# Kernel optimization log

Measured on AMD Instinct MI355X. Metric: run time of the kernel, lower is better.

The kernel has to match this reference:

```python
import jax, jax.numpy as jnp
import numpy as np

TEMPERATURE = 1.0
NUM_EXPERTS = 8


def setup_inputs() -> dict:
    key = jax.random.key(0)
    ks = jax.random.split(key, 7)
    B, S, H, E = 4, 4096, 1024, NUM_EXPERTS
    scale = 1.0 / np.sqrt(H)
    return {
        "hidden_states": jax.random.normal(ks[0], (B, S, H), dtype=jnp.float32),
        "w1": jax.random.normal(ks[1], (H, H // 2), dtype=jnp.float32) * scale,
        "b1": jax.random.normal(ks[2], (H // 2,), dtype=jnp.float32) * 0.01,
        "w2": jax.random.normal(ks[3], (H // 2, E), dtype=jnp.float32) * (1.0 / np.sqrt(H // 2)),
        "b2": jax.random.normal(ks[4], (E,), dtype=jnp.float32) * 0.01,
        "expert_W": jax.random.normal(ks[5], (E, H, H), dtype=jnp.float32) * scale,
        "expert_b": jax.random.normal(ks[6], (E, H), dtype=jnp.float32) * 0.01,
    }


def reference(hidden_states, w1, b1, w2, b2, expert_W, expert_b):
    # Router MLP: Linear(H, H//2) -> ReLU -> Linear(H//2, E)  (dropout inactive at eval)
    h = jax.nn.relu(jnp.einsum("bsh,hm->bsm", hidden_states, w1) + b1)
    routing_scores = (jnp.einsum("bsm,me->bse", h, w2) + b2) / TEMPERATURE
    expert_probs = jax.nn.softmax(routing_scores, axis=-1)
    # top-1 routing (topk with k=1 == argmax of probs)
    top_idx = jnp.argmax(expert_probs, axis=-1)  # [B, S]
    onehot = jax.nn.one_hot(top_idx, NUM_EXPERTS, dtype=hidden_states.dtype)  # [B, S, E]

    # _apply_expert_routing: for each expert, masked input -> dense transform -> masked accumulate
    routed = jnp.zeros_like(hidden_states)
    for e in range(NUM_EXPERTS):
        mask = onehot[..., e:e + 1]  # [B, S, 1]
        expert_out = jnp.einsum("bsh,hd->bsd", hidden_states * mask, expert_W[e]) + expert_b[e]
        routed = routed + expert_out * mask
    return routed
```

## Files before the change

### kernel.cpp

```cpp
#include <hip/hip_runtime.h>

#define NTOK 16384
#define HDIM 1024
#define MDIM 512
#define NEXP 8
#define CHUNK 128
#define MAXCHUNK 136
#define RCAP 4096
#define DELTA 0.02f
#define LSTR 72

#define G1_NWG ((MDIM / 128) * (NTOK / 128))
#define EG_NWG (8 * MAXCHUNK)

typedef __bf16 bf16x8 __attribute__((ext_vector_type(8)));
typedef float floatx4 __attribute__((ext_vector_type(4)));

__device__ __forceinline__ void gll16(const void* g, void* l) {
  __builtin_amdgcn_global_load_lds(
      (const __attribute__((address_space(1))) void*)g,
      (__attribute__((address_space(3))) void*)l, 16, 0, 0);
}

__global__ __launch_bounds__(256) void cvt_hs(
    const float* __restrict__ src, __bf16* __restrict__ dst)
{
  const size_t i = ((size_t)blockIdx.x * 256 + threadIdx.x) * 8;
  float4 a = *(const float4*)&src[i];
  float4 b = *(const float4*)&src[i + 4];
  bf16x8 o;
  o[0] = (__bf16)a.x; o[1] = (__bf16)a.y; o[2] = (__bf16)a.z; o[3] = (__bf16)a.w;
  o[4] = (__bf16)b.x; o[5] = (__bf16)b.y; o[6] = (__bf16)b.z; o[7] = (__bf16)b.w;
  *(bf16x8*)&dst[i] = o;
}

__global__ __launch_bounds__(256) void transpose_cvt(
    const float* __restrict__ src, __bf16* __restrict__ dst, int K, int C)
{
  __shared__ __align__(16) __bf16 T[64 * LSTR];
  const int b = blockIdx.z;
  const int k0 = blockIdx.x * 64, c0 = blockIdx.y * 64;
  const float* S = src + (size_t)b * K * C;
  __bf16* D = dst + (size_t)b * K * C;
  const int t = threadIdx.x;
  {
    const int r = t >> 2, cc = (t & 3) * 16;
    const float* p = S + (size_t)(k0 + r) * C + c0 + cc;
    float4 v0 = *(const float4*)&p[0];
    float4 v1 = *(const float4*)&p[4];
    float4 v2 = *(const float4*)&p[8];
    float4 v3 = *(const float4*)&p[12];
    float vv[16] = {v0.x, v0.y, v0.z, v0.w, v1.x, v1.y, v1.z, v1.w,
                    v2.x, v2.y, v2.z, v2.w, v3.x, v3.y, v3.z, v3.w};
#pragma unroll
    for (int j = 0; j < 16; ++j) T[(cc + j) * LSTR + r] = (__bf16)vv[j];
  }
  __syncthreads();
  {
    const int c = t >> 2, kk = (t & 3) * 16;
    __bf16* q = D + (size_t)(c0 + c) * K + k0 + kk;
    *(float4*)&q[0] = *(const float4*)&T[c * LSTR + kk];
    *(float4*)&q[8] = *(const float4*)&T[c * LSTR + kk + 8];
  }
}

__global__ __launch_bounds__(256) void gemm1_score(
    const __bf16* __restrict__ A,
    const __bf16* __restrict__ Bt,
    const float* __restrict__ bias,
    const float* __restrict__ w2,
    float* __restrict__ scores_part)
{
  __shared__ __align__(16) __bf16 As[2 * 128 * 64];
  __shared__ __align__(16) __bf16 Bs[2 * 128 * 64];

  const int tid = threadIdx.x;
  const int swz = (blockIdx.x & 7) * (G1_NWG / 8) + (blockIdx.x >> 3);
  const int rowBlk = swz >> 2;
  const int cb = swz & 3;
  const int row0 = rowBlk * 128, col0 = cb * 128;
  const int wave = tid >> 6, lane = tid & 63;
  const int lrow8 = lane >> 3;
  const int gchunk = (lane & 7) ^ lrow8;
  const int wr = (wave >> 1) * 64, wc = (wave & 1) * 64;
  const int lrow = lane & 15, quad = lane >> 4;

  const __bf16 *pa[4], *pb[4];
#pragma unroll
  for (int p = 0; p < 4; ++p) {
    const int rb = wave * 8 + p * 32;
    pa[p] = A + (size_t)(row0 + rb + lrow8) * HDIM + gchunk * 8;
    pb[p] = Bt + (size_t)(col0 + rb + lrow8) * HDIM + gchunk * 8;
  }

  floatx4 acc[4][4];
#pragma unroll
  for (int i = 0; i < 4; ++i)
#pragma unroll
    for (int j = 0; j < 4; ++j) acc[i][j] = (floatx4){0.f, 0.f, 0.f, 0.f};

#pragma unroll
  for (int p = 0; p < 4; ++p) {
    const int rb = wave * 8 + p * 32;
    gll16(pa[p], &As[rb * 64]);
    gll16(pb[p], &Bs[rb * 64]);
  }
  __syncthreads();

  int cur = 0;
  for (int t = 0; t < HDIM / 64; ++t) {
    const int nxt = cur ^ 1;
    if (t + 1 < HDIM / 64) {
      const int koff = (t + 1) * 64;
#pragma unroll
      for (int p = 0; p < 4; ++p) {
        const int rb = wave * 8 + p * 32;
        gll16(pa[p] + koff, &As[nxt * 8192 + rb * 64]);
        gll16(pb[p] + koff, &Bs[nxt * 8192 + rb * 64]);
      }
    }
    const __bf16* Ab = &As[cur * 8192];
    const __bf16* Bb = &Bs[cur * 8192];
#pragma unroll
    for (int kh = 0; kh < 2; ++kh) {
      bf16x8 a[4], b[4];
#pragma unroll
      for (int i = 0; i < 4; ++i)
        a[i] = *(const bf16x8*)&Ab[(wr + i * 16 + lrow) * 64 +
                                   (((kh * 4 + quad) ^ (lrow & 7)) * 8)];
#pragma unroll
      for (int j = 0; j < 4; ++j)
        b[j] = *(const bf16x8*)&Bb[(wc + j * 16 + lrow) * 64 +
                                   (((kh * 4 + quad) ^ (lrow & 7)) * 8)];
#pragma unroll
      for (int i = 0; i < 4; ++i)
#pragma unroll
        for (int j = 0; j < 4; ++j)
          acc[i][j] = __builtin_amdgcn_mfma_f32_16x16x32_bf16(a[i], b[j], acc[i][j], 0, 0, 0);
    }
    __syncthreads();
    cur = nxt;
  }

  float* w2s = (float*)As;
  float* sblk = (float*)Bs;
  *(float4*)&w2s[tid * 4] = *(const float4*)&w2[col0 * 8 + tid * 4];
  __syncthreads();

  float bj[4];
  float4 wja[4], wjb[4];
#pragma unroll
  for (int j = 0; j < 4; ++j) {
    const int cl = wc + j * 16 + lrow;
    bj[j] = bias[col0 + cl];
    wja[j] = *(const float4*)&w2s[cl * 8];
    wjb[j] = *(const float4*)&w2s[cl * 8 + 4];
  }

#pragma unroll
  for (int i = 0; i < 4; ++i) {
#pragma unroll
    for (int r = 0; r < 4; ++r) {
      float4 sA = {0, 0, 0, 0}, sB = {0, 0, 0, 0};
#pragma unroll
      for (int j = 0; j < 4; ++j) {
        float h = fmaxf(acc[i][j][r] + bj[j], 0.f);
        sA.x += h * wja[j].x; sA.y += h * wja[j].y;
        sA.z += h * wja[j].z; sA.w += h * wja[j].w;
        sB.x += h * wjb[j].x; sB.y += h * wjb[j].y;
        sB.z += h * wjb[j].z; sB.w += h * wjb[j].w;
      }
#pragma unroll
      for (int m = 1; m <= 8; m <<= 1) {
        sA.x += __shfl_xor(sA.x, m, 64); sA.y += __shfl_xor(sA.y, m, 64);
        sA.z += __shfl_xor(sA.z, m, 64); sA.w += __shfl_xor(sA.w, m, 64);
        sB.x += __shfl_xor(sB.x, m, 64); sB.y += __shfl_xor(sB.y, m, 64);
        sB.z += __shfl_xor(sB.z, m, 64); sB.w += __shfl_xor(sB.w, m, 64);
      }
      if (lrow == 0) {
        const int rloc = wr + i * 16 + quad * 4 + r;
        *(float4*)&sblk[((wave & 1) * 128 + rloc) * 8] = sA;
        *(float4*)&sblk[((wave & 1) * 128 + rloc) * 8 + 4] = sB;
      }
    }
  }
  __syncthreads();
  {
    const int r = tid >> 1, e4 = (tid & 1) * 4;
    float4 v0 = *(const float4*)&sblk[r * 8 + e4];
    float4 v1 = *(const float4*)&sblk[(128 + r) * 8 + e4];
    float4 o = {v0.x + v1.x, v0.y + v1.y, v0.z + v1.z, v0.w + v1.w};
    *(float4*)&scores_part[((size_t)cb * NTOK + row0 + r) * 8 + e4] = o;
  }
}

__global__ __launch_bounds__(256) void routing_argmax(
    const float* __restrict__ scores_part, const float* __restrict__ b2,
    int* __restrict__ top_idx, int* __restrict__ risky_n,
    int* __restrict__ risky)
{
  __shared__ int rbuf[256];
  __shared__ int rcnt, rbase;
  if (threadIdx.x == 0) rcnt = 0;
  __syncthreads();

  const int t = blockIdx.x * 256 + threadIdx.x;
  float4 sa = {0, 0, 0, 0}, sb = {0, 0, 0, 0};
#pragma unroll
  for (int c = 0; c < 4; ++c) {
    float4 va = *(const float4*)&scores_part[((size_t)c * NTOK + t) * 8];
    float4 vb = *(const float4*)&scores_part[((size_t)c * NTOK + t) * 8 + 4];
    sa.x += va.x; sa.y += va.y; sa.z += va.z; sa.w += va.w;
    sb.x += vb.x; sb.y += vb.y; sb.z += vb.z; sb.w += vb.w;
  }
  float s[8] = {sa.x + b2[0], sa.y + b2[1], sa.z + b2[2], sa.w + b2[3],
                sb.x + b2[4], sb.y + b2[5], sb.z + b2[6], sb.w + b2[7]};
  float best = s[0], second = -1e30f;
  int bi = 0;
#pragma unroll
  for (int e = 1; e < 8; ++e) {
    if (s[e] > best) { second = best; best = s[e]; bi = e; }
    else if (s[e] > second) second = s[e];
  }
  top_idx[t] = bi;
  if (best - second < DELTA) rbuf[atomicAdd(&rcnt, 1)] = t;
  __syncthreads();
  if (threadIdx.x == 0 && rcnt > 0) rbase = atomicAdd(risky_n, rcnt);
  __syncthreads();
  if ((int)threadIdx.x < rcnt) {
    int slot = rbase + threadIdx.x;
    if (slot < RCAP) risky[slot] = rbuf[threadIdx.x];
  }
}

__global__ __launch_bounds__(256) void gemm1_fix_v2(
    const float* __restrict__ A, const float* __restrict__ W,
    const float* __restrict__ bias, const int* __restrict__ risky,
    float* __restrict__ hfix)
{
  __shared__ float As[32][33];
  __shared__ float Bs[32][64];
  __shared__ int toks[32];

  const int tid = threadIdx.x;
  if (tid < 32) toks[tid] = risky[blockIdx.y * 32 + tid];
  __syncthreads();
  if (toks[0] < 0) return;

  const int col0 = blockIdx.x * 64;
  const int tx = tid & 15, ty = tid >> 4;
  float acc0[4] = {0, 0, 0, 0}, acc1[4] = {0, 0, 0, 0};

  const int sr = tid >> 3;
  const int sc4 = (tid & 3) * 8;
  const int lo = tid & 7;
  const int sc8 = lo * 8;
  const int tokS = toks[sr];
  const float* pa = (tokS >= 0) ? A + (size_t)tokS * HDIM : A;

  for (int k0 = 0; k0 < HDIM; k0 += 32) {
    float4 av = make_float4(0, 0, 0, 0);
    if (tokS >= 0) av = *(const float4*)&pa[k0 + (lo & 3) * 4 + (lo >> 2) * 16];
    float4 b0 = *(const float4*)&W[(size_t)(k0 + sr) * MDIM + col0 + sc8];
    float4 b1v = *(const float4*)&W[(size_t)(k0 + sr) * MDIM + col0 + sc8 + 4];
    const int kk = (lo & 3) * 4 + (lo >> 2) * 16;
    As[kk + 0][sr] = av.x; As[kk + 1][sr] = av.y;
    As[kk + 2][sr] = av.z; As[kk + 3][sr] = av.w;
    (void)sc4;
    *(float4*)&Bs[sr][sc8] = b0;
    *(float4*)&Bs[sr][sc8 + 4] = b1v;
    __syncthreads();

#pragma unroll
    for (int k = 0; k < 32; ++k) {
      float a0 = As[k][ty], a1 = As[k][ty + 16];
      float4 bv = *(const float4*)&Bs[k][tx * 4];
      acc0[0] = fmaf(a0, bv.x, acc0[0]); acc0[1] = fmaf(a0, bv.y, acc0[1]);
      acc0[2] = fmaf(a0, bv.z, acc0[2]); acc0[3] = fmaf(a0, bv.w, acc0[3]);
      acc1[0] = fmaf(a1, bv.x, acc1[0]); acc1[1] = fmaf(a1, bv.y, acc1[1]);
      acc1[2] = fmaf(a1, bv.z, acc1[2]); acc1[3] = fmaf(a1, bv.w, acc1[3]);
    }
    __syncthreads();
  }

  const int c = col0 + tx * 4;
  const int i0 = blockIdx.y * 32 + ty, i1 = blockIdx.y * 32 + ty + 16;
  if (toks[ty] >= 0) {
    float4 v;
    v.x = fmaxf(acc0[0] + bias[c + 0], 0.f); v.y = fmaxf(acc0[1] + bias[c + 1], 0.f);
    v.z = fmaxf(acc0[2] + bias[c + 2], 0.f); v.w = fmaxf(acc0[3] + bias[c + 3], 0.f);
    *(float4*)&hfix[(size_t)i0 * MDIM + c] = v;
  }
  if (toks[ty + 16] >= 0) {
    float4 v;
    v.x = fmaxf(acc1[0] + bias[c + 0], 0.f); v.y = fmaxf(acc1[1] + bias[c + 1], 0.f);
    v.z = fmaxf(acc1[2] + bias[c + 2], 0.f); v.w = fmaxf(acc1[3] + bias[c + 3], 0.f);
    *(float4*)&hfix[(size_t)i1 * MDIM + c] = v;
  }
}

__global__ __launch_bounds__(256) void rescore_fix(
    const float* __restrict__ hfix, const float* __restrict__ w2,
    const float* __restrict__ b2, const int* __restrict__ risky,
    int* __restrict__ top_idx)
{
  const int idx = blockIdx.x * 32 + (threadIdx.x >> 3);
  const int l8 = threadIdx.x & 7;
  const int t = risky[idx];

  float s[8] = {0, 0, 0, 0, 0, 0, 0, 0};
  if (t >= 0) {
    const float* hrow = hfix + (size_t)idx * MDIM;
    for (int k = l8; k < MDIM; k += 8) {
      float hv = hrow[k];
      float4 wa = *(const float4*)&w2[k * 8];
      float4 wb = *(const float4*)&w2[k * 8 + 4];
      s[0] += hv * wa.x; s[1] += hv * wa.y; s[2] += hv * wa.z; s[3] += hv * wa.w;
      s[4] += hv * wb.x; s[5] += hv * wb.y; s[6] += hv * wb.z; s[7] += hv * wb.w;
    }
  }
#pragma unroll
  for (int off = 4; off > 0; off >>= 1)
#pragma unroll
    for (int e = 0; e < 8; ++e) s[e] += __shfl_xor(s[e], off, 64);

  if (l8 == 0 && t >= 0) {
    float best = s[0] + b2[0];
    int bi = 0;
#pragma unroll
    for (int e = 1; e < 8; ++e) {
      float v = s[e] + b2[e];
      if (v > best) { best = v; bi = e; }
    }
    top_idx[t] = bi;
  }
}

__global__ __launch_bounds__(256) void count_tokens(
    const int* __restrict__ top_idx, int* __restrict__ counts)
{
  __shared__ int lc[NEXP];
  if (threadIdx.x < NEXP) lc[threadIdx.x] = 0;
  __syncthreads();
  atomicAdd(&lc[top_idx[blockIdx.x * 256 + threadIdx.x]], 1);
  __syncthreads();
  if (threadIdx.x < NEXP) atomicAdd(&counts[threadIdx.x], lc[threadIdx.x]);
}

__global__ __launch_bounds__(256) void scatter_tokens(
    const int* __restrict__ top_idx, const int* __restrict__ counts,
    int* __restrict__ cursor, int* __restrict__ sorted)
{
  __shared__ int lc[NEXP], lbase[NEXP], off_s[NEXP];
  if (threadIdx.x < NEXP) lc[threadIdx.x] = 0;
  if (threadIdx.x == 0) {
    int off = 0;
    for (int e = 0; e < NEXP; ++e) {
      off_s[e] = off;
      off += ((counts[e] + CHUNK - 1) / CHUNK) * CHUNK;
    }
  }
  __syncthreads();
  const int t = blockIdx.x * 256 + threadIdx.x;
  const int e = top_idx[t];
  const int r = atomicAdd(&lc[e], 1);
  __syncthreads();
  if (threadIdx.x < NEXP)
    lbase[threadIdx.x] = atomicAdd(&cursor[threadIdx.x], lc[threadIdx.x]);
  __syncthreads();
  sorted[off_s[e] + lbase[e] + r] = t;
}

__global__ __launch_bounds__(256) void expert_gemm_v4(
    const __bf16* __restrict__ A,
    const __bf16* __restrict__ Wt,
    const float* __restrict__ Eb,
    const int* __restrict__ sorted,
    const int* __restrict__ top_idx,
    float* __restrict__ Out)
{
  __shared__ __align__(16) __bf16 As[2 * 128 * 64];
  __shared__ __align__(16) __bf16 Bs[2 * 128 * 64];
  __shared__ int toks[CHUNK];

  const int tid = threadIdx.x;
  const int swz = (blockIdx.x & 7) * (EG_NWG / 8) + (blockIdx.x >> 3);
  const int chunkIdx = swz >> 3;
  const int cb = swz & 7;
  if (tid < CHUNK) toks[tid] = sorted[(size_t)chunkIdx * CHUNK + tid];
  __syncthreads();
  if (toks[0] < 0) return;

  const int e = top_idx[toks[0]];
  const int col0 = cb * 128;
  const int wave = tid >> 6, lane = tid & 63;
  const int lrow8 = lane >> 3;
  const int gchunk = (lane & 7) ^ lrow8;
  const int wr = (wave >> 1) * 64, wc = (wave & 1) * 64;
  const int lrow = lane & 15, quad = lane >> 4;

  const __bf16 *pa[4], *pb[4];
#pragma unroll
  for (int p = 0; p < 4; ++p) {
    const int rb = wave * 8 + p * 32;
    const int tk = toks[rb + lrow8];
    pa[p] = A + (size_t)(tk < 0 ? 0 : tk) * HDIM + gchunk * 8;
    pb[p] = Wt + ((size_t)e * HDIM + col0 + rb + lrow8) * HDIM + gchunk * 8;
  }

  floatx4 acc[4][4];
#pragma unroll
  for (int i = 0; i < 4; ++i)
#pragma unroll
    for (int j = 0; j < 4; ++j) acc[i][j] = (floatx4){0.f, 0.f, 0.f, 0.f};

#pragma unroll
  for (int p = 0; p < 4; ++p) {
    const int rb = wave * 8 + p * 32;
    gll16(pa[p], &As[rb * 64]);
    gll16(pb[p], &Bs[rb * 64]);
  }
  __syncthreads();

  int cur = 0;
  for (int t = 0; t < HDIM / 64; ++t) {
    const int nxt = cur ^ 1;
    if (t + 1 < HDIM / 64) {
      const int koff = (t + 1) * 64;
#pragma unroll
      for (int p = 0; p < 4; ++p) {
        const int rb = wave * 8 + p * 32;
        gll16(pa[p] + koff, &As[nxt * 8192 + rb * 64]);
        gll16(pb[p] + koff, &Bs[nxt * 8192 + rb * 64]);
      }
    }
    const __bf16* Ab = &As[cur * 8192];
    const __bf16* Bb = &Bs[cur * 8192];
#pragma unroll
    for (int kh = 0; kh < 2; ++kh) {
      bf16x8 a[4], b[4];
#pragma unroll
      for (int i = 0; i < 4; ++i)
        a[i] = *(const bf16x8*)&Ab[(wr + i * 16 + lrow) * 64 +
                                   (((kh * 4 + quad) ^ (lrow & 7)) * 8)];
#pragma unroll
      for (int j = 0; j < 4; ++j)
        b[j] = *(const bf16x8*)&Bb[(wc + j * 16 + lrow) * 64 +
                                   (((kh * 4 + quad) ^ (lrow & 7)) * 8)];
#pragma unroll
      for (int i = 0; i < 4; ++i)
#pragma unroll
        for (int j = 0; j < 4; ++j)
          acc[i][j] = __builtin_amdgcn_mfma_f32_16x16x32_bf16(a[i], b[j], acc[i][j], 0, 0, 0);
    }
    __syncthreads();
    cur = nxt;
  }

  const float* be = Eb + (size_t)e * HDIM + col0;
#pragma unroll
  for (int i = 0; i < 4; ++i)
#pragma unroll
    for (int r = 0; r < 4; ++r) {
      const int row = wr + i * 16 + quad * 4 + r;
      const int tok = toks[row];
      if (tok < 0) continue;
      float* po = Out + (size_t)tok * HDIM + col0;
#pragma unroll
      for (int j = 0; j < 4; ++j) {
        const int col = wc + j * 16 + lrow;
        po[col] = acc[i][j][r] + be[col];
      }
    }
}

extern "C" void kernel_launch(void* const* d_in, const int* in_sizes, int n_in,
                              void* d_out, int out_size, void* d_ws, size_t ws_size,
                              hipStream_t stream) {
  (void)in_sizes; (void)n_in; (void)out_size; (void)ws_size;

  const float* hs = (const float*)d_in[0];
  const float* w1 = (const float*)d_in[1];
  const float* b1 = (const float*)d_in[2];
  const float* w2 = (const float*)d_in[3];
  const float* b2 = (const float*)d_in[4];
  const float* eW = (const float*)d_in[5];
  const float* eb = (const float*)d_in[6];
  float* out = (float*)d_out;

  float* hfix = (float*)d_out;
  float* scores_part = hfix + (size_t)RCAP * MDIM;

  char* wsb = (char*)d_ws;
  int* top_idx = (int*)wsb;
  int* ctrl    = (int*)(wsb + 65536);
  int* counts  = ctrl;
  int* risky_n = ctrl + 8;
  int* cursor  = ctrl + 16;
  int* risky   = (int*)(wsb + 65792);
  int* sorted  = risky + RCAP;
  __bf16* hs_bf = (__bf16*)(wsb + 163840);
  __bf16* w1t   = (__bf16*)(wsb + 163840 + 33554432);
  __bf16* eWt   = (__bf16*)(wsb + 163840 + 33554432 + 1048576);

  hipMemsetAsync(ctrl, 0, 128, stream);
  hipMemsetAsync(risky, 0xFF, (RCAP + MAXCHUNK * CHUNK) * sizeof(int), stream);

  cvt_hs<<<NTOK * HDIM / (256 * 8), 256, 0, stream>>>(hs, hs_bf);
  transpose_cvt<<<dim3(HDIM / 64, MDIM / 64, 1), 256, 0, stream>>>(w1, w1t, HDIM, MDIM);
  transpose_cvt<<<dim3(HDIM / 64, HDIM / 64, NEXP), 256, 0, stream>>>(eW, eWt, HDIM, HDIM);

  gemm1_score<<<dim3(G1_NWG), 256, 0, stream>>>(hs_bf, w1t, b1, w2, scores_part);
  routing_argmax<<<NTOK / 256, 256, 0, stream>>>(scores_part, b2, top_idx, risky_n, risky);
  gemm1_fix_v2<<<dim3(MDIM / 64, RCAP / 32), 256, 0, stream>>>(hs, w1, b1, risky, hfix);
  rescore_fix<<<RCAP / 32, 256, 0, stream>>>(hfix, w2, b2, risky, top_idx);
  count_tokens<<<NTOK / 256, 256, 0, stream>>>(top_idx, counts);
  scatter_tokens<<<NTOK / 256, 256, 0, stream>>>(top_idx, counts, cursor, sorted);
  expert_gemm_v4<<<dim3(EG_NWG), 256, 0, stream>>>(hs_bf, eWt, eb, sorted, top_idx, out);
}
```

Before: 326.0 us.

## Deepen GEMM pipelines to 4-stage with 512-thread blocks and split router scoring

Both bf16 GEMMs (router layer 1 and expert GEMM) move from 256-thread double-buffered tiles to 512-thread blocks with a 4-buffer LDS ring, prefetching three K-steps ahead. They use explicit vmcnt waits and a single barrier per step in place of two syncthreads. The router's fused ReLU·w2 epilogue is removed: gemm1 now writes bf16 hidden activations to scratch, and a new score_route kernel computes the scores and argmax per token. This targets memory latency and epilogue reduction cost, but adds a bf16 round-trip of the hidden activations and 128KB of LDS per block, which limits occupancy. The extra rounding of h to bf16 may shift which tokens fall in the near-tie set.

```diff
diff --git a/kernel.cpp b/kernel.cpp
--- a/kernel.cpp
+++ b/kernel.cpp
@@ -9,6 +9,7 @@
 #define RCAP 4096
 #define DELTA 0.02f
 #define LSTR 72
+#define NSTEP 16
 
 #define G1_NWG ((MDIM / 128) * (NTOK / 128))
 #define EG_NWG (8 * MAXCHUNK)
@@ -64,15 +65,14 @@
   }
 }
 
-__global__ __launch_bounds__(256) void gemm1_score(
+__global__ __launch_bounds__(512, 2) void gemm1_h(
     const __bf16* __restrict__ A,
     const __bf16* __restrict__ Bt,
     const float* __restrict__ bias,
-    const float* __restrict__ w2,
-    float* __restrict__ scores_part)
-{
-  __shared__ __align__(16) __bf16 As[2 * 128 * 64];
-  __shared__ __align__(16) __bf16 Bs[2 * 128 * 64];
+    __bf16* __restrict__ hbf)
+{
+  __shared__ __align__(16) __bf16 As[4][128 * 64];
+  __shared__ __align__(16) __bf16 Bs[4][128 * 64];
 
   const int tid = threadIdx.x;
   const int swz = (blockIdx.x & 7) * (G1_NWG / 8) + (blockIdx.x >> 3);
@@ -82,148 +82,135 @@
   const int wave = tid >> 6, lane = tid & 63;
   const int lrow8 = lane >> 3;
   const int gchunk = (lane & 7) ^ lrow8;
-  const int wr = (wave >> 1) * 64, wc = (wave & 1) * 64;
+  const int wr = (wave >> 2) * 64;
+  const int wc = (wave & 3) * 32;
   const int lrow = lane & 15, quad = lane >> 4;
 
-  const __bf16 *pa[4], *pb[4];
-#pragma unroll
-  for (int p = 0; p < 4; ++p) {
-    const int rb = wave * 8 + p * 32;
+  const __bf16 *pa[2], *pb[2];
+#pragma unroll
+  for (int p = 0; p < 2; ++p) {
+    const int rb = wave * 8 + p * 64;
     pa[p] = A + (size_t)(row0 + rb + lrow8) * HDIM + gchunk * 8;
     pb[p] = Bt + (size_t)(col0 + rb + lrow8) * HDIM + gchunk * 8;
   }
 
-  floatx4 acc[4][4];
+  floatx4 acc[4][2];
 #pragma unroll
   for (int i = 0; i < 4; ++i)
 #pragma unroll
-    for (int j = 0; j < 4; ++j) acc[i][j] = (floatx4){0.f, 0.f, 0.f, 0.f};
-
-#pragma unroll
-  for (int p = 0; p < 4; ++p) {
-    const int rb = wave * 8 + p * 32;
-    gll16(pa[p], &As[rb * 64]);
-    gll16(pb[p], &Bs[rb * 64]);
-  }
-  __syncthreads();
-
-  int cur = 0;
-  for (int t = 0; t < HDIM / 64; ++t) {
-    const int nxt = cur ^ 1;
-    if (t + 1 < HDIM / 64) {
-      const int koff = (t + 1) * 64;
-#pragma unroll
-      for (int p = 0; p < 4; ++p) {
-        const int rb = wave * 8 + p * 32;
-        gll16(pa[p] + koff, &As[nxt * 8192 + rb * 64]);
-        gll16(pb[p] + koff, &Bs[nxt * 8192 + rb * 64]);
+    for (int j = 0; j < 2; ++j) acc[i][j] = (floatx4){0.f, 0.f, 0.f, 0.f};
+
+#pragma unroll
+  for (int pt = 0; pt < 3; ++pt) {
+#pragma unroll
+    for (int p = 0; p < 2; ++p) {
+      const int rb = wave * 8 + p * 64;
+      gll16(pa[p] + pt * 64, &As[pt][rb * 64]);
+      gll16(pb[p] + pt * 64, &Bs[pt][rb * 64]);
+    }
+  }
+
+  for (int t = 0; t < NSTEP; ++t) {
+    if (t < NSTEP - 2)      asm volatile("s_waitcnt vmcnt(8)" ::: "memory");
+    else if (t == NSTEP - 2) asm volatile("s_waitcnt vmcnt(4)" ::: "memory");
+    else                     asm volatile("s_waitcnt vmcnt(0)" ::: "memory");
+    __builtin_amdgcn_s_barrier();
+    __builtin_amdgcn_sched_barrier(0);
+    if (t + 3 < NSTEP) {
+      const int koff = (t + 3) * 64;
+      const int bn = (t + 3) & 3;
+#pragma unroll
+      for (int p = 0; p < 2; ++p) {
+        const int rb = wave * 8 + p * 64;
+        gll16(pa[p] + koff, &As[bn][rb * 64]);
+        gll16(pb[p] + koff, &Bs[bn][rb * 64]);
       }
     }
-    const __bf16* Ab = &As[cur * 8192];
-    const __bf16* Bb = &Bs[cur * 8192];
+    __builtin_amdgcn_sched_barrier(0);
+    const __bf16* Ab = As[t & 3];
+    const __bf16* Bb = Bs[t & 3];
 #pragma unroll
     for (int kh = 0; kh < 2; ++kh) {
-      bf16x8 a[4], b[4];
+      bf16x8 a[4], b[2];
 #pragma unroll
       for (int i = 0; i < 4; ++i)
         a[i] = *(const bf16x8*)&Ab[(wr + i * 16 + lrow) * 64 +
                                    (((kh * 4 + quad) ^ (lrow & 7)) * 8)];
 #pragma unroll
-      for (int j = 0; j < 4; ++j)
+      for (int j = 0; j < 2; ++j)
         b[j] = *(const bf16x8*)&Bb[(wc + j * 16 + lrow) * 64 +
                                    (((kh * 4 + quad) ^ (lrow & 7)) * 8)];
 #pragma unroll
       for (int i = 0; i < 4; ++i)
 #pragma unroll
-        for (int j = 0; j < 4; ++j)
+        for (int j = 0; j < 2; ++j)
           acc[i][j] = __builtin_amdgcn_mfma_f32_16x16x32_bf16(a[i], b[j], acc[i][j], 0, 0, 0);
     }
-    __syncthreads();
-    cur = nxt;
-  }
-
-  float* w2s = (float*)As;
-  float* sblk = (float*)Bs;
-  *(float4*)&w2s[tid * 4] = *(const float4*)&w2[col0 * 8 + tid * 4];
-  __syncthreads();
-
-  float bj[4];
-  float4 wja[4], wjb[4];
-#pragma unroll
-  for (int j = 0; j < 4; ++j) {
-    const int cl = wc + j * 16 + lrow;
-    bj[j] = bias[col0 + cl];
-    wja[j] = *(const float4*)&w2s[cl * 8];
-    wjb[j] = *(const float4*)&w2s[cl * 8 + 4];
-  }
-
-#pragma unroll
-  for (int i = 0; i < 4; ++i) {
+  }
+
+  float bj[2];
+#pragma unroll
+  for (int j = 0; j < 2; ++j) bj[j] = bias[col0 + wc + j * 16 + lrow];
+#pragma unroll
+  for (int i = 0; i < 4; ++i)
 #pragma unroll
     for (int r = 0; r < 4; ++r) {
-      float4 sA = {0, 0, 0, 0}, sB = {0, 0, 0, 0};
-#pragma unroll
-      for (int j = 0; j < 4; ++j) {
-        float h = fmaxf(acc[i][j][r] + bj[j], 0.f);
-        sA.x += h * wja[j].x; sA.y += h * wja[j].y;
-        sA.z += h * wja[j].z; sA.w += h * wja[j].w;
-        sB.x += h * wjb[j].x; sB.y += h * wjb[j].y;
-        sB.z += h * wjb[j].z; sB.w += h * wjb[j].w;
+      const int tokr = row0 + wr + i * 16 + quad * 4 + r;
+      __bf16* hp = hbf + (size_t)tokr * MDIM + col0;
+#pragma unroll
+      for (int j = 0; j < 2; ++j) {
+        const int cl = wc + j * 16 + lrow;
+        hp[cl] = (__bf16)fmaxf(acc[i][j][r] + bj[j], 0.f);
       }
-#pragma unroll
-      for (int m = 1; m <= 8; m <<= 1) {
-        sA.x += __shfl_xor(sA.x, m, 64); sA.y += __shfl_xor(sA.y, m, 64);
-        sA.z += __shfl_xor(sA.z, m, 64); sA.w += __shfl_xor(sA.w, m, 64);
-        sB.x += __shfl_xor(sB.x, m, 64); sB.y += __shfl_xor(sB.y, m, 64);
-        sB.z += __shfl_xor(sB.z, m, 64); sB.w += __shfl_xor(sB.w, m, 64);
-      }
-      if (lrow == 0) {
-        const int rloc = wr + i * 16 + quad * 4 + r;
-        *(float4*)&sblk[((wave & 1) * 128 + rloc) * 8] = sA;
-        *(float4*)&sblk[((wave & 1) * 128 + rloc) * 8 + 4] = sB;
-      }
-    }
-  }
-  __syncthreads();
-  {
-    const int r = tid >> 1, e4 = (tid & 1) * 4;
-    float4 v0 = *(const float4*)&sblk[r * 8 + e4];
-    float4 v1 = *(const float4*)&sblk[(128 + r) * 8 + e4];
-    float4 o = {v0.x + v1.x, v0.y + v1.y, v0.z + v1.z, v0.w + v1.w};
-    *(float4*)&scores_part[((size_t)cb * NTOK + row0 + r) * 8 + e4] = o;
-  }
-}
-
-__global__ __launch_bounds__(256) void routing_argmax(
-    const float* __restrict__ scores_part, const float* __restrict__ b2,
-    int* __restrict__ top_idx, int* __restrict__ risky_n,
-    int* __restrict__ risky)
-{
-  __shared__ int rbuf[256];
+    }
+}
+
+__global__ __launch_bounds__(256) void score_route(
+    const __bf16* __restrict__ hbf, const float* __restrict__ w2,
+    const float* __restrict__ b2, int* __restrict__ top_idx,
+    int* __restrict__ risky_n, int* __restrict__ risky)
+{
+  __shared__ int rbuf[32];
   __shared__ int rcnt, rbase;
   if (threadIdx.x == 0) rcnt = 0;
   __syncthreads();
 
-  const int t = blockIdx.x * 256 + threadIdx.x;
-  float4 sa = {0, 0, 0, 0}, sb = {0, 0, 0, 0};
-#pragma unroll
-  for (int c = 0; c < 4; ++c) {
-    float4 va = *(const float4*)&scores_part[((size_t)c * NTOK + t) * 8];
-    float4 vb = *(const float4*)&scores_part[((size_t)c * NTOK + t) * 8 + 4];
-    sa.x += va.x; sa.y += va.y; sa.z += va.z; sa.w += va.w;
-    sb.x += vb.x; sb.y += vb.y; sb.z += vb.z; sb.w += vb.w;
-  }
-  float s[8] = {sa.x + b2[0], sa.y + b2[1], sa.z + b2[2], sa.w + b2[3],
-                sb.x + b2[4], sb.y + b2[5], sb.z + b2[6], sb.w + b2[7]};
-  float best = s[0], second = -1e30f;
-  int bi = 0;
-#pragma unroll
-  for (int e = 1; e < 8; ++e) {
-    if (s[e] > best) { second = best; best = s[e]; bi = e; }
-    else if (s[e] > second) second = s[e];
-  }
-  top_idx[t] = bi;
-  if (best - second < DELTA) rbuf[atomicAdd(&rcnt, 1)] = t;
+  const int tok = blockIdx.x * 32 + (threadIdx.x >> 3);
+  const int l8 = threadIdx.x & 7;
+  const __bf16* hrow = hbf + (size_t)tok * MDIM;
+
+  float s[8] = {0, 0, 0, 0, 0, 0, 0, 0};
+#pragma unroll
+  for (int u = 0; u < 8; ++u) {
+    const int m0 = u * 64 + l8 * 8;
+    bf16x8 hv = *(const bf16x8*)&hrow[m0];
+#pragma unroll
+    for (int q = 0; q < 8; ++q) {
+      const float h = (float)hv[q];
+      float4 wa = *(const float4*)&w2[(m0 + q) * 8];
+      float4 wb = *(const float4*)&w2[(m0 + q) * 8 + 4];
+      s[0] += h * wa.x; s[1] += h * wa.y; s[2] += h * wa.z; s[3] += h * wa.w;
+      s[4] += h * wb.x; s[5] += h * wb.y; s[6] += h * wb.z; s[7] += h * wb.w;
+    }
+  }
+#pragma unroll
+  for (int off = 1; off <= 4; off <<= 1)
+#pragma unroll
+    for (int e = 0; e < 8; ++e) s[e] += __shfl_xor(s[e], off, 64);
+
+  if (l8 == 0) {
+    float v0 = s[0] + b2[0];
+    float best = v0, second = -1e30f;
+    int bi = 0;
+#pragma unroll
+    for (int e = 1; e < 8; ++e) {
+      float v = s[e] + b2[e];
+      if (v > best) { second = best; best = v; bi = e; }
+      else if (v > second) second = v;
+    }
+    top_idx[tok] = bi;
+    if (best - second < DELTA) rbuf[atomicAdd(&rcnt, 1)] = tok;
+  }
   __syncthreads();
   if (threadIdx.x == 0 && rcnt > 0) rbase = atomicAdd(risky_n, rcnt);
   __syncthreads();
@@ -252,7 +239,6 @@
   float acc0[4] = {0, 0, 0, 0}, acc1[4] = {0, 0, 0, 0};
 
   const int sr = tid >> 3;
-  const int sc4 = (tid & 3) * 8;
   const int lo = tid & 7;
   const int sc8 = lo * 8;
   const int tokS = toks[sr];
@@ -266,7 +252,6 @@
     const int kk = (lo & 3) * 4 + (lo >> 2) * 16;
     As[kk + 0][sr] = av.x; As[kk + 1][sr] = av.y;
     As[kk + 2][sr] = av.z; As[kk + 3][sr] = av.w;
-    (void)sc4;
     *(float4*)&Bs[sr][sc8] = b0;
     *(float4*)&Bs[sr][sc8 + 4] = b1v;
     __syncthreads();
@@ -371,7 +356,7 @@
   sorted[off_s[e] + lbase[e] + r] = t;
 }
 
-__global__ __launch_bounds__(256) void expert_gemm_v4(
+__global__ __launch_bounds__(512, 2) void expert_gemm_v5(
     const __bf16* __restrict__ A,
     const __bf16* __restrict__ Wt,
     const float* __restrict__ Eb,
@@ -379,8 +364,8 @@
     const int* __restrict__ top_idx,
     float* __restrict__ Out)
 {
-  __shared__ __align__(16) __bf16 As[2 * 128 * 64];
-  __shared__ __align__(16) __bf16 Bs[2 * 128 * 64];
+  __shared__ __align__(16) __bf16 As[4][128 * 64];
+  __shared__ __align__(16) __bf16 Bs[4][128 * 64];
   __shared__ int toks[CHUNK];
 
   const int tid = threadIdx.x;
@@ -396,65 +381,71 @@
   const int wave = tid >> 6, lane = tid & 63;
   const int lrow8 = lane >> 3;
   const int gchunk = (lane & 7) ^ lrow8;
-  const int wr = (wave >> 1) * 64, wc = (wave & 1) * 64;
+  const int wr = (wave >> 2) * 64;
+  const int wc = (wave & 3) * 32;
   const int lrow = lane & 15, quad = lane >> 4;
 
-  const __bf16 *pa[4], *pb[4];
-#pragma unroll
-  for (int p = 0; p < 4; ++p) {
-    const int rb = wave * 8 + p * 32;
+  const __bf16 *pa[2], *pb[2];
+#pragma unroll
+  for (int p = 0; p < 2; ++p) {
+    const int rb = wave * 8 + p * 64;
     const int tk = toks[rb + lrow8];
     pa[p] = A + (size_t)(tk < 0 ? 0 : tk) * HDIM + gchunk * 8;
     pb[p] = Wt + ((size_t)e * HDIM + col0 + rb + lrow8) * HDIM + gchunk * 8;
   }
 
-  floatx4 acc[4][4];
+  floatx4 acc[4][2];
 #pragma unroll
   for (int i = 0; i < 4; ++i)
 #pragma unroll
-    for (int j = 0; j < 4; ++j) acc[i][j] = (floatx4){0.f, 0.f, 0.f, 0.f};
-
-#pragma unroll
-  for (int p = 0; p < 4; ++p) {
-    const int rb = wave * 8 + p * 32;
-    gll16(pa[p], &As[rb * 64]);
-    gll16(pb[p], &Bs[rb * 64]);
-  }
-  __syncthreads();
-
-  int cur = 0;
-  for (int t = 0; t < HDIM / 64; ++t) {
-    const int nxt = cur ^ 1;
-    if (t + 1 < HDIM / 64) {
-      const int koff = (t + 1) * 64;
-#pragma unroll
-      for (int p = 0; p < 4; ++p) {
-        const int rb = wave * 8 + p * 32;
-        gll16(pa[p] + koff, &As[nxt * 8192 + rb * 64]);
-        gll16(pb[p] + koff, &Bs[nxt * 8192 + rb * 64]);
+    for (int j = 0; j < 2; ++j) acc[i][j] = (floatx4){0.f, 0.f, 0.f, 0.f};
+
+#pragma unroll
+  for (int pt = 0; pt < 3; ++pt) {
+#pragma unroll
+    for (int p = 0; p < 2; ++p) {
+      const int rb = wave * 8 + p * 64;
+      gll16(pa[p] + pt * 64, &As[pt][rb * 64]);
+      gll16(pb[p] + pt * 64, &Bs[pt][rb * 64]);
+    }
+  }
+
+  for (int t = 0; t < NSTEP; ++t) {
+    if (t < NSTEP - 2)      asm volatile("s_waitcnt vmcnt(8)" ::: "memory");
+    else if (t == NSTEP - 2) asm volatile("s_waitcnt vmcnt(4)" ::: "memory");
+    else                     asm volatile("s_waitcnt vmcnt(0)" ::: "memory");
+    __builtin_amdgcn_s_barrier();
+    __builtin_amdgcn_sched_barrier(0);
+    if (t + 3 < NSTEP) {
+      const int koff = (t + 3) * 64;
+      const int bn = (t + 3) & 3;
+#pragma unroll
+      for (int p = 0; p < 2; ++p) {
+        const int rb = wave * 8 + p * 64;
+        gll16(pa[p] + koff, &As[bn][rb * 64]);
+        gll16(pb[p] + koff, &Bs[bn][rb * 64]);
       }
     }
-    const __bf16* Ab = &As[cur * 8192];
-    const __bf16* Bb = &Bs[cur * 8192];
+    __builtin_amdgcn_sched_barrier(0);
+    const __bf16* Ab = As[t & 3];
+    const __bf16* Bb = Bs[t & 3];
 #pragma unroll
     for (int kh = 0; kh < 2; ++kh) {
-      bf16x8 a[4], b[4];
+      bf16x8 a[4], b[2];
 #pragma unroll
       for (int i = 0; i < 4; ++i)
         a[i] = *(const bf16x8*)&Ab[(wr + i * 16 + lrow) * 64 +
                                    (((kh * 4 + quad) ^ (lrow & 7)) * 8)];
 #pragma unroll
-      for (int j = 0; j < 4; ++j)
+      for (int j = 0; j < 2; ++j)
         b[j] = *(const bf16x8*)&Bb[(wc + j * 16 + lrow) * 64 +
                                    (((kh * 4 + quad) ^ (lrow & 7)) * 8)];
 #pragma unroll
       for (int i = 0; i < 4; ++i)
 #pragma unroll
-        for (int j = 0; j < 4; ++j)
+        for (int j = 0; j < 2; ++j)
           acc[i][j] = __builtin_amdgcn_mfma_f32_16x16x32_bf16(a[i], b[j], acc[i][j], 0, 0, 0);
     }
-    __syncthreads();
-    cur = nxt;
   }
 
   const float* be = Eb + (size_t)e * HDIM + col0;
@@ -467,7 +458,7 @@
       if (tok < 0) continue;
       float* po = Out + (size_t)tok * HDIM + col0;
 #pragma unroll
-      for (int j = 0; j < 4; ++j) {
+      for (int j = 0; j < 2; ++j) {
         const int col = wc + j * 16 + lrow;
         po[col] = acc[i][j][r] + be[col];
       }
@@ -489,7 +480,7 @@
   float* out = (float*)d_out;
 
   float* hfix = (float*)d_out;
-  float* scores_part = hfix + (size_t)RCAP * MDIM;
+  __bf16* h_bf = (__bf16*)((char*)d_out + (size_t)8 * 1024 * 1024);
 
   char* wsb = (char*)d_ws;
   int* top_idx = (int*)wsb;
@@ -510,11 +501,11 @@
   transpose_cvt<<<dim3(HDIM / 64, MDIM / 64, 1), 256, 0, stream>>>(w1, w1t, HDIM, MDIM);
   transpose_cvt<<<dim3(HDIM / 64, HDIM / 64, NEXP), 256, 0, stream>>>(eW, eWt, HDIM, HDIM);
 
-  gemm1_score<<<dim3(G1_NWG), 256, 0, stream>>>(hs_bf, w1t, b1, w2, scores_part);
-  routing_argmax<<<NTOK / 256, 256, 0, stream>>>(scores_part, b2, top_idx, risky_n, risky);
+  gemm1_h<<<dim3(G1_NWG), 512, 0, stream>>>(hs_bf, w1t, b1, h_bf);
+  score_route<<<NTOK / 32, 256, 0, stream>>>(h_bf, w2, b2, top_idx, risky_n, risky);
   gemm1_fix_v2<<<dim3(MDIM / 64, RCAP / 32), 256, 0, stream>>>(hs, w1, b1, risky, hfix);
   rescore_fix<<<RCAP / 32, 256, 0, stream>>>(hfix, w2, b2, risky, top_idx);
   count_tokens<<<NTOK / 256, 256, 0, stream>>>(top_idx, counts);
   scatter_tokens<<<NTOK / 256, 256, 0, stream>>>(top_idx, counts, cursor, sorted);
-  expert_gemm_v4<<<dim3(EG_NWG), 256, 0, stream>>>(hs_bf, eWt, eb, sorted, top_idx, out);
-}
+  expert_gemm_v5<<<dim3(EG_NWG), 512, 0, stream>>>(hs_bf, eWt, eb, sorted, top_idx, out);
+}
```

Result: slower. 382.7 us (+17.4%).
